# Performance work log

Measured on AMD Instinct MI355X. Metric: run time of the kernel, lower is better.

Reference implementation:

```python
import jax, jax.numpy as jnp
import numpy as np

B, D, H = 4096, 64, 512  # batch, event dim, MLP hidden


def _net(z, t, W1, b1, W2, b2, W3, b3):
    # z: [..., D]; t: scalar, broadcast as a time feature column
    tcol = jnp.broadcast_to(t, z.shape[:-1] + (1,))
    x = jnp.concatenate([z, tcol], axis=-1)            # [..., D+1]
    h = jnp.tanh(x @ W1 + b1)                          # [..., H]
    h = jnp.tanh(h @ W2 + b2)                          # [..., H]
    return h @ W3 + b3                                 # [..., D]


def setup_inputs() -> dict:
    key = jax.random.key(0)
    ks = jax.random.split(key, 6)
    s_in = 1.0 / np.sqrt(D + 1)
    s_h = 1.0 / np.sqrt(H)
    return {
        "z": jax.random.normal(ks[0], (B, D), dtype=jnp.float32),
        "log_pz": jnp.zeros((B, 1), dtype=jnp.float32),
        "t": jax.random.uniform(ks[1], (1,), dtype=jnp.float32),
        "W1": jax.random.normal(ks[2], (D + 1, H), dtype=jnp.float32) * s_in,
        "b1": jnp.zeros((H,), dtype=jnp.float32),
        "W2": jax.random.normal(ks[3], (H, H), dtype=jnp.float32) * s_h,
        "b2": jnp.zeros((H,), dtype=jnp.float32),
        "W3": jax.random.normal(ks[4], (H, D), dtype=jnp.float32) * s_h,
        "b3": jnp.zeros((D,), dtype=jnp.float32),
    }


def reference(z, log_pz, t, W1, b1, W2, b2, W3, b3):
    tval = t[0]
    # velocity field v = net(z, t), batched
    v = _net(z, tval, W1, b1, W2, b2, W3, b3)          # [B, D]
    # exact Jacobian trace: replaces the torch per-dim autograd.grad loop
    # with a fully vectorized per-sample forward-mode Jacobian.
    f_single = lambda zi: _net(zi, tval, W1, b1, W2, b2, W3, b3)  # [D] -> [D]
    jac = jax.vmap(jax.jacfwd(f_single))(z)            # [B, D, D]
    dlogp_dt = -jnp.trace(jac, axis1=1, axis2=2)[:, None]  # [B, 1]
    return (v, dlogp_dt)
```

## Files before the change

kernel.cpp:

```cpp
#include <hip/hip_runtime.h>
#include <hip/hip_bf16.h>

#define BB 4096
#define DD 64
#define HH 512

typedef short short8 __attribute__((ext_vector_type(8)));
typedef float f32x4  __attribute__((ext_vector_type(4)));
typedef __hip_bfloat16 bf16;

__device__ __forceinline__ float tanh_fast(float x) {
    float e = __expf(2.0f * x);
    return 1.0f - __fdividef(2.0f, 1.0f + e);
}

__device__ __forceinline__ void st_swz(bf16* base, int row, int col, int rs, float v) {
    base[row * rs + ((((col >> 3) ^ (row & 7))) << 3) + (col & 7)] = __float2bfloat16(v);
}

#define GLD1(dst, addr)                                                      \
  asm volatile("global_load_dwordx4 %0, %1, off" : "=&v"(dst) : "v"(addr))

#define GLD2(e0, e1, addr)                                                   \
  asm volatile("global_load_dwordx4 %0, %2, off\n\t"                         \
               "global_load_dwordx4 %1, %2, off offset:1024"                 \
               : "=&v"(e0), "=&v"(e1) : "v"(addr))

#define GLD4(e0, e1, e2, e3, addr)                                           \
  asm volatile("global_load_dwordx4 %0, %4, off\n\t"                         \
               "global_load_dwordx4 %1, %4, off offset:1024\n\t"             \
               "global_load_dwordx4 %2, %4, off offset:2048\n\t"             \
               "global_load_dwordx4 %3, %4, off offset:3072"                 \
               : "=&v"(e0), "=&v"(e1), "=&v"(e2), "=&v"(e3) : "v"(addr))

#define WAITV(n)                                                             \
  do { asm volatile("s_waitcnt vmcnt(" #n ")" ::: "memory");                 \
       __builtin_amdgcn_sched_barrier(0); } while (0)

__global__ __launch_bounds__(256) void prep_kernel(
    const float* __restrict__ t, const float* __restrict__ W1,
    const float* __restrict__ b1, const float* __restrict__ W2,
    const float* __restrict__ W3, const float* __restrict__ b3,
    bf16* __restrict__ W1p, bf16* __restrict__ W2p, bf16* __restrict__ W3p,
    bf16* __restrict__ Pp, float* __restrict__ b1eff, float* __restrict__ out)
{
    const int tid  = threadIdx.x;
    const int bx   = blockIdx.x;
    const int lane = tid & 63;
    const int r    = lane & 15;
    const int kq   = lane >> 4;

    if (bx < 160) {
        int T = bx * 4 + (tid >> 6);
        const float* src;
        bf16* dst;
        int stride;
        if (T < 64) {
            int w = T >> 2, s = (T >> 1) & 1, f = T & 1;
            src = W1 + (size_t)(s * 32 + kq * 8) * HH + (w * 2 + f) * 16 + r;
            stride = HH;
            dst = W1p + (size_t)T * 512 + lane * 8;
        } else if (T < 576) {
            int tt = T - 64;
            int cw = tt >> 4, s = tt & 15;
            src = W2 + (size_t)(s * 32 + kq * 8) * HH + cw * 16 + r;
            stride = HH;
            dst = W2p + (size_t)tt * 512 + lane * 8;
        } else {
            int tt = T - 576;
            int q = tt >> 2, f = tt & 3;
            src = W3 + (size_t)(q * 32 + kq * 8) * DD + f * 16 + r;
            stride = DD;
            dst = W3p + (size_t)tt * 512 + lane * 8;
        }
        short8 v;
#pragma unroll
        for (int j = 0; j < 8; ++j)
            v[j] = (short)__bfloat16_as_ushort(__float2bfloat16(src[(size_t)j * stride]));
        *(short8*)dst = v;
    } else if (bx < 288) {
        int pt = (bx - 160) * 4 + (tid >> 6);
        int cw = pt >> 4, s = pt & 15;
        int k  = cw * 16 + r;
        int j0 = s * 32 + kq * 8;
        float acc[8] = {};
        const float* w3row = W3 + (size_t)k * DD;
        for (int d = 0; d < DD; ++d) {
            float w3 = w3row[d];
            const float4* w1p4 = (const float4*)(W1 + (size_t)d * HH + j0);
            float4 x = w1p4[0], y = w1p4[1];
            acc[0] += x.x * w3; acc[1] += x.y * w3;
            acc[2] += x.z * w3; acc[3] += x.w * w3;
            acc[4] += y.x * w3; acc[5] += y.y * w3;
            acc[6] += y.z * w3; acc[7] += y.w * w3;
        }
        short8 v;
#pragma unroll
        for (int j = 0; j < 8; ++j)
            v[j] = (short)__bfloat16_as_ushort(
                __float2bfloat16(acc[j] * W2[(size_t)(j0 + j) * HH + k]));
        *(short8*)(Pp + (size_t)pt * 512 + lane * 8) = v;
    } else if (bx == 288) {
        float tv = t[0];
        b1eff[tid]       = b1[tid]       + tv * W1[(size_t)64 * HH + tid];
        b1eff[tid + 256] = b1[tid + 256] + tv * W1[(size_t)64 * HH + tid + 256];
    } else {
        int idx = (bx - 289) * 1024 + tid * 4;
        if (idx < BB * DD) {
            int col = idx & 63;
            *(float4*)(out + idx) =
                make_float4(b3[col], b3[col + 1], b3[col + 2], b3[col + 3]);
        } else {
            *(float4*)(out + idx) = make_float4(0.f, 0.f, 0.f, 0.f);
        }
    }
}

__global__ __launch_bounds__(1024, 2) void fused_rows(
    const float* __restrict__ z, const bf16* __restrict__ W1p,
    const bf16* __restrict__ W2p, const bf16* __restrict__ W3p,
    const bf16* __restrict__ Pp, const float* __restrict__ b1eff,
    const float* __restrict__ b2,
    float* __restrict__ outV, float* __restrict__ outTr)
{
    __shared__ alignas(16) char smem[88064];
    bf16* zt   = (bf16*)smem;
    bf16* h1   = (bf16*)(smem + 4096);
    bf16* at   = (bf16*)(smem + 36864);
    bf16* h2   = (bf16*)(smem + 69632);
    float* trp = (float*)(smem + 86016);
    float* vp  = (float*)smem;

    const int tid  = threadIdx.x;
    const int wid  = tid >> 6;
    const int lane = tid & 63;
    const int r    = lane & 15;
    const int kq   = lane >> 4;
    const int rx   = r & 7;
    const int laneE = lane * 8;
    const int rt   = blockIdx.x >> 1;
    const int ch   = blockIdx.x & 1;
    const int bm   = rt * 32;

    float bias1[2];
#pragma unroll
    for (int f = 0; f < 2; ++f) bias1[f] = b1eff[wid * 32 + f * 16 + r];
    float bias2 = b2[ch * 256 + wid * 16 + r];
    asm volatile("" :: "v"(bias1[0]), "v"(bias1[1]), "v"(bias2));

    {
        int i = tid * 2;
        int row = i >> 6, col = i & 63;
        float2 v = *(const float2*)(z + (size_t)(bm + row) * DD + col);
        st_swz(zt, row, col,     64, v.x);
        st_swz(zt, row, col + 1, 64, v.y);
    }

    short8 q0, q1, q2, q3, p0, p1;
    const bf16* Wb1 = W1p + (size_t)wid * 2048 + laneE;
    GLD2(q0, q1, Wb1);
    GLD2(p0, p1, Wb1 + 1024);
    __syncthreads();

    f32x4 acc1[2][2] = {};
    WAITV(2);
#pragma unroll
    for (int g = 0; g < 2; ++g) {
        short8 av = *(const short8*)(zt + (g * 16 + r) * 64 + ((kq ^ rx) << 3));
        acc1[g][0] = __builtin_amdgcn_mfma_f32_16x16x32_bf16(av, q0, acc1[g][0], 0, 0, 0);
        acc1[g][1] = __builtin_amdgcn_mfma_f32_16x16x32_bf16(av, q1, acc1[g][1], 0, 0, 0);
    }
    WAITV(0);
#pragma unroll
    for (int g = 0; g < 2; ++g) {
        short8 av = *(const short8*)(zt + (g * 16 + r) * 64 + (((4 + kq) ^ rx) << 3));
        acc1[g][0] = __builtin_amdgcn_mfma_f32_16x16x32_bf16(av, p0, acc1[g][0], 0, 0, 0);
        acc1[g][1] = __builtin_amdgcn_mfma_f32_16x16x32_bf16(av, p1, acc1[g][1], 0, 0, 0);
    }
    short8 rb[3];
    const bf16* Wb2 = W2p + (size_t)(ch * 16 + wid) * 8192 + laneE;
    GLD1(rb[0], Wb2);
    GLD1(rb[1], Wb2 + 512);
#pragma unroll
    for (int g = 0; g < 2; ++g)
#pragma unroll
        for (int f = 0; f < 2; ++f) {
            int col = wid * 32 + f * 16 + r;
#pragma unroll
            for (int v = 0; v < 4; ++v) {
                int row = g * 16 + kq * 4 + v;
                float h = tanh_fast(acc1[g][f][v] + bias1[f]);
                st_swz(h1, row, col, 512, h);
                st_swz(at, row, col, 512, fmaf(-h, h, 1.0f));
            }
        }
    __syncthreads();

    f32x4 bsq[2];
    {
        f32x4 acc2[2] = {};
#pragma unroll
        for (int s = 0; s < 16; ++s) {
            if (s + 2 < 16)      { GLD1(rb[(s + 2) % 3], Wb2 + (s + 2) * 512); WAITV(2); }
            else if (s + 1 < 16) { WAITV(1); }
            else                 { WAITV(0); }
#pragma unroll
            for (int g = 0; g < 2; ++g) {
                short8 av = *(const short8*)(h1 + (g * 16 + r) * 512 + (((s * 4 + kq) ^ rx) << 3));
                acc2[g] = __builtin_amdgcn_mfma_f32_16x16x32_bf16(av, rb[s % 3], acc2[g], 0, 0, 0);
            }
        }
        const bf16* WbE = Pp + (size_t)(ch * 16 + wid) * 8192 + laneE;
        GLD1(rb[0], WbE);
        GLD1(rb[1], WbE + 512);
        int colL = wid * 16 + r;
#pragma unroll
        for (int g = 0; g < 2; ++g)
#pragma unroll
            for (int v = 0; v < 4; ++v) {
                int row = g * 16 + kq * 4 + v;
                float h = tanh_fast(acc2[g][v] + bias2);
                st_swz(h2, row, colL, 256, h);
                bsq[g][v] = fmaf(-h, h, 1.0f);
            }
    }

    {
        const bf16* WbE = Pp + (size_t)(ch * 16 + wid) * 8192 + laneE;
        f32x4 accE[2] = {};
#pragma unroll
        for (int s = 0; s < 16; ++s) {
            if (s + 2 < 16)      { GLD1(rb[(s + 2) % 3], WbE + (s + 2) * 512); WAITV(2); }
            else if (s + 1 < 16) { WAITV(1); }
            else                 { WAITV(0); }
#pragma unroll
            for (int g = 0; g < 2; ++g) {
                short8 av = *(const short8*)(at + (g * 16 + r) * 512 + (((s * 4 + kq) ^ rx) << 3));
                accE[g] = __builtin_amdgcn_mfma_f32_16x16x32_bf16(av, rb[s % 3], accE[g], 0, 0, 0);
            }
        }
        const int kw = wid & 7;
        const bf16* Wb3 = W3p + (size_t)(ch * 8 + kw) * 2048 + laneE;
        GLD4(q0, q1, q2, q3, Wb3);
#pragma unroll
        for (int g = 0; g < 2; ++g)
#pragma unroll
            for (int v = 0; v < 4; ++v) {
                float p = accE[g][v] * bsq[g][v];
                p += __shfl_xor(p, 1);
                p += __shfl_xor(p, 2);
                p += __shfl_xor(p, 4);
                p += __shfl_xor(p, 8);
                if (r == 0) trp[wid * 32 + g * 16 + kq * 4 + v] = p;
            }
    }
    __syncthreads();

    {
        const int kw = wid & 7, rp = wid >> 3;
        f32x4 c0 = {}, c1 = {}, c2 = {}, c3 = {};
        WAITV(0);
        short8 av = *(const short8*)(h2 + (rp * 16 + r) * 256 + (((kw * 4 + kq) ^ rx) << 3));
        c0 = __builtin_amdgcn_mfma_f32_16x16x32_bf16(av, q0, c0, 0, 0, 0);
        c1 = __builtin_amdgcn_mfma_f32_16x16x32_bf16(av, q1, c1, 0, 0, 0);
        c2 = __builtin_amdgcn_mfma_f32_16x16x32_bf16(av, q2, c2, 0, 0, 0);
        c3 = __builtin_amdgcn_mfma_f32_16x16x32_bf16(av, q3, c3, 0, 0, 0);
#pragma unroll
        for (int v = 0; v < 4; ++v) {
            int row = rp * 16 + kq * 4 + v;
            vp[kw * 2048 + row * 64 + 0 * 16 + r] = c0[v];
            vp[kw * 2048 + row * 64 + 1 * 16 + r] = c1[v];
            vp[kw * 2048 + row * 64 + 2 * 16 + r] = c2[v];
            vp[kw * 2048 + row * 64 + 3 * 16 + r] = c3[v];
        }
    }
    __syncthreads();

#pragma unroll
    for (int it = 0; it < 2; ++it) {
        int i = it * 1024 + tid;
        int row = i >> 6, col = i & 63;
        float s = 0.f;
#pragma unroll
        for (int kw = 0; kw < 8; ++kw) s += vp[kw * 2048 + i];
        atomicAdd(outV + (size_t)(bm + row) * DD + col, s);
    }
    if (tid < 32) {
        float s = 0.f;
#pragma unroll
        for (int w = 0; w < 16; ++w) s += trp[w * 32 + tid];
        atomicAdd(outTr + bm + tid, -s);
    }
}

extern "C" void kernel_launch(void* const* d_in, const int* in_sizes, int n_in,
                              void* d_out, int out_size, void* d_ws, size_t ws_size,
                              hipStream_t stream)
{
    const float* z  = (const float*)d_in[0];
    const float* t  = (const float*)d_in[2];
    const float* W1 = (const float*)d_in[3];
    const float* b1 = (const float*)d_in[4];
    const float* W2 = (const float*)d_in[5];
    const float* b2 = (const float*)d_in[6];
    const float* W3 = (const float*)d_in[7];
    const float* b3 = (const float*)d_in[8];
    float* out = (float*)d_out;
    float* out_tr = out + (size_t)BB * DD;

    char* w = (char*)d_ws;
    auto alloc = [&](size_t bytes) {
        char* p = w;
        w += (bytes + 255) & ~(size_t)255;
        return p;
    };
    bf16* W1p   = (bf16*)alloc((size_t)64  * 512 * 2);
    bf16* W2p   = (bf16*)alloc((size_t)512 * 512 * 2);
    bf16* W3p   = (bf16*)alloc((size_t)64  * 512 * 2);
    bf16* Pp    = (bf16*)alloc((size_t)512 * 512 * 2);
    float* b1eff = (float*)alloc((size_t)HH * 4);

    prep_kernel<<<549, 256, 0, stream>>>(t, W1, b1, W2, W3, b3,
                                         W1p, W2p, W3p, Pp, b1eff, out);
    fused_rows<<<128 * 2, 1024, 0, stream>>>(z, W1p, W2p, W3p, Pp,
                                             b1eff, b2, out, out_tr);
}
```

Before: 27.06 us.

## Fuse layer-2 and Jacobian-trace GEMM loops with deeper prefetch and lighter barriers

Merges the two sequential K-loops (h1·W2 and the derivative-path GEMM against Pp) into a single loop that issues both weight streams together, using a 4-deep register ring buffer per stream instead of a 3-deep shared one. It also replaces __syncthreads with a custom barrier that waits only on LDS counters, so outstanding global prefetches are not drained at barriers. The h2 LDS read is moved ahead of the vmcnt wait. The intent is to hide global load latency and expose more independent MFMAs per step, at the cost of higher VGPR use and a custom barrier that depends on correct hand-placed wait counts.

```diff
diff --git a/kernel.cpp b/kernel.cpp
--- a/kernel.cpp
+++ b/kernel.cpp
@@ -35,6 +35,11 @@
 
 #define WAITV(n)                                                             \
   do { asm volatile("s_waitcnt vmcnt(" #n ")" ::: "memory");                 \
+       __builtin_amdgcn_sched_barrier(0); } while (0)
+
+#define LGKMBAR()                                                            \
+  do { asm volatile("s_waitcnt lgkmcnt(0)" ::: "memory");                    \
+       __builtin_amdgcn_s_barrier();                                         \
        __builtin_amdgcn_sched_barrier(0); } while (0)
 
 __global__ __launch_bounds__(256) void prep_kernel(
@@ -160,7 +165,7 @@
     const bf16* Wb1 = W1p + (size_t)wid * 2048 + laneE;
     GLD2(q0, q1, Wb1);
     GLD2(p0, p1, Wb1 + 1024);
-    __syncthreads();
+    LGKMBAR();
 
     f32x4 acc1[2][2] = {};
     WAITV(2);
@@ -177,10 +182,12 @@
         acc1[g][0] = __builtin_amdgcn_mfma_f32_16x16x32_bf16(av, p0, acc1[g][0], 0, 0, 0);
         acc1[g][1] = __builtin_amdgcn_mfma_f32_16x16x32_bf16(av, p1, acc1[g][1], 0, 0, 0);
     }
-    short8 rb[3];
+    short8 rbW[4], rbP[4];
     const bf16* Wb2 = W2p + (size_t)(ch * 16 + wid) * 8192 + laneE;
-    GLD1(rb[0], Wb2);
-    GLD1(rb[1], Wb2 + 512);
+    const bf16* WbE = Pp  + (size_t)(ch * 16 + wid) * 8192 + laneE;
+    GLD1(rbW[0], Wb2);        GLD1(rbP[0], WbE);
+    GLD1(rbW[1], Wb2 + 512);  GLD1(rbP[1], WbE + 512);
+    GLD1(rbW[2], Wb2 + 1024); GLD1(rbP[2], WbE + 1024);
 #pragma unroll
     for (int g = 0; g < 2; ++g)
 #pragma unroll
@@ -194,25 +201,34 @@
                 st_swz(at, row, col, 512, fmaf(-h, h, 1.0f));
             }
         }
-    __syncthreads();
-
+    LGKMBAR();
+
+    f32x4 acc2[2] = {};
+    f32x4 accE[2] = {};
+#pragma unroll
+    for (int s = 0; s < 16; ++s) {
+        int co = (((s * 4 + kq) ^ rx) << 3);
+        short8 a1v[2], aav[2];
+#pragma unroll
+        for (int g = 0; g < 2; ++g) {
+            a1v[g] = *(const short8*)(h1 + (g * 16 + r) * 512 + co);
+            aav[g] = *(const short8*)(at + (g * 16 + r) * 512 + co);
+        }
+        if (s + 3 < 16) {
+            GLD1(rbW[(s + 3) & 3], Wb2 + (s + 3) * 512);
+            GLD1(rbP[(s + 3) & 3], WbE + (s + 3) * 512);
+            WAITV(6);
+        } else if (s + 2 < 16) { WAITV(4); }
+        else if (s + 1 < 16)   { WAITV(2); }
+        else                   { WAITV(0); }
+#pragma unroll
+        for (int g = 0; g < 2; ++g) {
+            acc2[g] = __builtin_amdgcn_mfma_f32_16x16x32_bf16(a1v[g], rbW[s & 3], acc2[g], 0, 0, 0);
+            accE[g] = __builtin_amdgcn_mfma_f32_16x16x32_bf16(aav[g], rbP[s & 3], accE[g], 0, 0, 0);
+        }
+    }
     f32x4 bsq[2];
     {
-        f32x4 acc2[2] = {};
-#pragma unroll
-        for (int s = 0; s < 16; ++s) {
-            if (s + 2 < 16)      { GLD1(rb[(s + 2) % 3], Wb2 + (s + 2) * 512); WAITV(2); }
-            else if (s + 1 < 16) { WAITV(1); }
-            else                 { WAITV(0); }
-#pragma unroll
-            for (int g = 0; g < 2; ++g) {
-                short8 av = *(const short8*)(h1 + (g * 16 + r) * 512 + (((s * 4 + kq) ^ rx) << 3));
-                acc2[g] = __builtin_amdgcn_mfma_f32_16x16x32_bf16(av, rb[s % 3], acc2[g], 0, 0, 0);
-            }
-        }
-        const bf16* WbE = Pp + (size_t)(ch * 16 + wid) * 8192 + laneE;
-        GLD1(rb[0], WbE);
-        GLD1(rb[1], WbE + 512);
         int colL = wid * 16 + r;
 #pragma unroll
         for (int g = 0; g < 2; ++g)
@@ -223,22 +239,6 @@
                 st_swz(h2, row, colL, 256, h);
                 bsq[g][v] = fmaf(-h, h, 1.0f);
             }
-    }
-
-    {
-        const bf16* WbE = Pp + (size_t)(ch * 16 + wid) * 8192 + laneE;
-        f32x4 accE[2] = {};
-#pragma unroll
-        for (int s = 0; s < 16; ++s) {
-            if (s + 2 < 16)      { GLD1(rb[(s + 2) % 3], WbE + (s + 2) * 512); WAITV(2); }
-            else if (s + 1 < 16) { WAITV(1); }
-            else                 { WAITV(0); }
-#pragma unroll
-            for (int g = 0; g < 2; ++g) {
-                short8 av = *(const short8*)(at + (g * 16 + r) * 512 + (((s * 4 + kq) ^ rx) << 3));
-                accE[g] = __builtin_amdgcn_mfma_f32_16x16x32_bf16(av, rb[s % 3], accE[g], 0, 0, 0);
-            }
-        }
         const int kw = wid & 7;
         const bf16* Wb3 = W3p + (size_t)(ch * 8 + kw) * 2048 + laneE;
         GLD4(q0, q1, q2, q3, Wb3);
@@ -254,13 +254,13 @@
                 if (r == 0) trp[wid * 32 + g * 16 + kq * 4 + v] = p;
             }
     }
-    __syncthreads();
+    LGKMBAR();
 
     {
         const int kw = wid & 7, rp = wid >> 3;
         f32x4 c0 = {}, c1 = {}, c2 = {}, c3 = {};
+        short8 av = *(const short8*)(h2 + (rp * 16 + r) * 256 + (((kw * 4 + kq) ^ rx) << 3));
         WAITV(0);
-        short8 av = *(const short8*)(h2 + (rp * 16 + r) * 256 + (((kw * 4 + kq) ^ rx) << 3));
         c0 = __builtin_amdgcn_mfma_f32_16x16x32_bf16(av, q0, c0, 0, 0, 0);
         c1 = __builtin_amdgcn_mfma_f32_16x16x32_bf16(av, q1, c1, 0, 0, 0);
         c2 = __builtin_amdgcn_mfma_f32_16x16x32_bf16(av, q2, c2, 0, 0, 0);
@@ -274,7 +274,7 @@
             vp[kw * 2048 + row * 64 + 3 * 16 + r] = c3[v];
         }
     }
-    __syncthreads();
+    LGKMBAR();
 
 #pragma unroll
     for (int it = 0; it < 2; ++it) {
```

Measured after the change: 26.57 us. Within noise of the previous version (-1.8%).
